# Kernel tuning notes

Hardware: AMD Instinct MI355X
Metric: run time of the kernel (lower is better)

The kernel has to match this reference:

```python
import jax, jax.numpy as jnp
import numpy as np


def conv3x3(x, w):
    # x: [B,C,H,W], w: [O,I,3,3], stride 1, pad 1, no bias
    return jax.lax.conv_general_dilated(
        x, w, window_strides=(1, 1), padding=[(1, 1), (1, 1)],
        dimension_numbers=("NCHW", "OIHW", "NCHW"))


def deform_conv2d(x, offset, w):
    """torchvision-style DeformConv2d: k=3, stride=1, pad=1, dilation=1,
    1 offset group, no bias. x:[B,C,H,W], offset:[B,18,H,W] (dy,dx pairs
    per kernel tap, k = kh*3+kw), w:[O,C,3,3]. Zero padding outside."""
    B, C, H, W = x.shape
    K = 9
    dy = offset[:, 0::2]  # [B,9,H,W]
    dx = offset[:, 1::2]
    kh = (jnp.arange(K) // 3 - 1).astype(x.dtype)[None, :, None, None]
    kw = (jnp.arange(K) % 3 - 1).astype(x.dtype)[None, :, None, None]
    hh = jnp.arange(H, dtype=x.dtype)[None, None, :, None]
    ww = jnp.arange(W, dtype=x.dtype)[None, None, None, :]
    py = hh + kh + dy  # sampling y coord, [B,9,H,W]
    px = ww + kw + dx
    y0 = jnp.floor(py)
    x0 = jnp.floor(px)
    wy = py - y0
    wx = px - x0
    x_hwc = jnp.transpose(x, (0, 2, 3, 1))  # [B,H,W,C]
    b_idx = jnp.arange(B)[:, None, None, None]

    def gather(yi, xi):
        valid = (yi >= 0) & (yi <= H - 1) & (xi >= 0) & (xi <= W - 1)
        yc = jnp.clip(yi, 0, H - 1).astype(jnp.int32)
        xc = jnp.clip(xi, 0, W - 1).astype(jnp.int32)
        v = x_hwc[b_idx, yc, xc]  # [B,9,H,W,C]
        return v * valid[..., None].astype(x.dtype)

    v00 = gather(y0, x0)
    v01 = gather(y0, x0 + 1)
    v10 = gather(y0 + 1, x0)
    v11 = gather(y0 + 1, x0 + 1)
    wy = wy[..., None]
    wx = wx[..., None]
    sampled = (v00 * (1 - wy) * (1 - wx) + v01 * (1 - wy) * wx
               + v10 * wy * (1 - wx) + v11 * wy * wx)  # [B,9,H,W,C]
    wk = w.reshape(w.shape[0], w.shape[1], K)  # [O,C,9]
    return jnp.einsum("bkhwc,ock->bohw", sampled, wk)


def setup_inputs() -> dict:
    key = jax.random.key(0)
    ks = jax.random.split(key, 6)
    B, C, H, W = 2, 128, 128, 128
    s = 0.05  # small init so learned offsets stay in a realistic range
    return {
        "input_features": jax.random.normal(ks[0], (B, C, H, W), jnp.float32),
        "reference_features": jax.random.normal(ks[1], (B, C, H, W), jnp.float32),
        "w_est1": jax.random.normal(ks[2], (C, 2 * C, 3, 3), jnp.float32) * s,
        "w_est2": jax.random.normal(ks[3], (C, C, 3, 3), jnp.float32) * s,
        "w_off": jax.random.normal(ks[4], (18, C, 3, 3), jnp.float32) * s,
        "w_def": jax.random.normal(ks[5], (C, C, 3, 3), jnp.float32) * s,
    }


def reference(input_features, reference_features, w_est1, w_est2, w_off, w_def):
    # concat input+reference features along channel dim
    feat = jnp.concatenate([input_features, reference_features], axis=1)  # [B,2C,H,W]
    # dynamic offset estimator: 2-layer 3x3 conv stack 2C->C->C with ReLU
    est = jax.nn.relu(conv3x3(feat, w_est1))
    est = jax.nn.relu(conv3x3(est, w_est2))
    # offset head: C -> 2*9 offsets per pixel
    offset = conv3x3(est, w_off)  # [B,18,H,W]
    # deformable conv over the reference features
    return deform_conv2d(reference_features, offset, w_def)
```

## Files before the change

kernel.cpp:

```cpp
#include <hip/hip_runtime.h>

typedef _Float16 f16;
typedef __attribute__((ext_vector_type(8))) _Float16 f16x8;
typedef __attribute__((ext_vector_type(4))) float f32x4;
typedef __attribute__((ext_vector_type(4))) int i32x4;


__device__ __forceinline__ void pack_conv(const float* __restrict__ src, f16* __restrict__ dst,
                                          long idx, int C) {
  int ci3 = idx & 7;
  int g = (idx >> 3) & 3;
  long t = idx >> 5;
  int o = (int)(t & 63); t >>= 6;
  int kx = (int)(t % 3); t /= 3;
  int nb = (int)(t & 1); t >>= 1;
  int nkc = C >> 5;
  int cc = (int)(t % nkc);
  int ky = (int)(t / nkc);
  int og = nb * 64 + o;
  int c = (cc << 5) + ((g ^ ((o >> 1) & 3)) << 3) + ci3;
  dst[idx] = (f16)src[(((size_t)og * C + c) * 3 + ky) * 3 + kx];
}

__device__ __forceinline__ void halo_zero(f16* __restrict__ buf, long e) {
  int c = (int)(e & 127);
  long t = e >> 7;
  int b = (int)(t / 516);
  int p = (int)(t % 516);
  int y, x;
  if (p < 130)      { y = 0;   x = p; }
  else if (p < 260) { y = 129; x = p - 130; }
  else if (p < 388) { x = 0;   y = p - 259; }
  else              { x = 129; y = p - 387; }
  buf[((size_t)(b * 130 + y) * 130 + x) * 128 + c] = (f16)0.f;
}

__global__ __launch_bounds__(256) void init_k(const float* __restrict__ x, const float* __restrict__ ref,
                                              const float* __restrict__ w1, const float* __restrict__ w2,
                                              const float* __restrict__ woff, const float* __restrict__ wdef,
                                              f16* __restrict__ W1p, f16* __restrict__ W2p,
                                              f16* __restrict__ Woffp, f16* __restrict__ Wdefp,
                                              f16* __restrict__ xP, f16* __restrict__ refP,
                                              f16* __restrict__ est1, f16* __restrict__ est2) {
  __shared__ __align__(16) f16 T[64][40];
  int tid = threadIdx.x;
  if (blockIdx.x < 4096) {
    int bi = blockIdx.x;
    int row = bi & 255, wseg = (bi >> 8) & 1, chunk = bi >> 9;
    int b = row >> 7, h = row & 127;
    int w0 = wseg * 64;
    const float* src = (chunk < 4) ? x : ref;
    f16* dstp = (chunk < 4) ? xP : refP;
    int c0 = (chunk & 3) * 32;
#pragma unroll
    for (int i = 0; i < 2; ++i) {
      int idx = tid + i * 256;
      int c = idx >> 4, g = idx & 15;
      const float4 v = *(const float4*)(src + (((size_t)(b * 128 + c0 + c)) * 128 + h) * 128 + w0 + g * 4);
      T[g * 4 + 0][c] = (f16)v.x;
      T[g * 4 + 1][c] = (f16)v.y;
      T[g * 4 + 2][c] = (f16)v.z;
      T[g * 4 + 3][c] = (f16)v.w;
    }
    __syncthreads();
    int w = tid >> 2, g = tid & 3;
    f16x8 o = *(const f16x8*)&T[w][g * 8];
    *(f16x8*)(dstp + ((size_t)(b * 130 + h + 1) * 130 + w0 + w + 1) * 128 + c0 + g * 8) = o;
    return;
  }
  long idx = (long)(blockIdx.x - 4096) * 256 + tid;
  if (idx < 294912) { pack_conv(w1, W1p, idx, 256); return; }
  idx -= 294912;
  if (idx < 147456) { pack_conv(w2, W2p, idx, 128); return; }
  idx -= 147456;
  if (idx < 36864) {
    int ci3 = (int)(idx & 7);
    int g = (int)((idx >> 3) & 3);
    int o = (int)((idx >> 5) & 31);
    int t2 = (int)(idx >> 10);
    int kx = t2 % 3; t2 /= 3;
    int cc = t2 & 3, ky = t2 >> 2;
    int c = (cc << 5) + ((g ^ ((o >> 1) & 3)) << 3) + ci3;
    Woffp[idx] = (o < 18) ? (f16)woff[(((size_t)o * 128 + c) * 3 + ky) * 3 + kx] : (f16)0.f;
    return;
  }
  idx -= 36864;
  if (idx < 147456) {
    int j = (int)(idx & 7);
    int ln = (int)((idx >> 3) & 63);
    int ofr = (int)((idx >> 9) & 7);
    int cc = (int)((idx >> 12) & 3);
    int t = (int)(idx >> 14);
    int o = ofr * 16 + (ln & 15);
    int c = cc * 32 + (ln >> 4) * 8 + j;
    Wdefp[idx] = (f16)wdef[(((size_t)o * 128 + c) * 3 + t / 3) * 3 + t % 3];
    return;
  }
  idx -= 147456;
  if (idx < 132096) { halo_zero(xP, idx); return; }
  idx -= 132096;
  if (idx < 132096) { halo_zero(refP, idx); return; }
  idx -= 132096;
  if (idx < 132096) { halo_zero(est1, idx); return; }
  idx -= 132096;
  if (idx < 132096) halo_zero(est2, idx);
}

template <int NKC>
__global__ __launch_bounds__(256, 2) void conv_k(const f16* __restrict__ src0,
                                                 const f16* __restrict__ src1,
                                                 const f16* __restrict__ Wp,
                                                 f16* __restrict__ dst) {
  constexpr int S = 3 * NKC;
  const int j = blockIdx.x;
  const int xcd = j & 7, ji = j >> 3;
  const int row = xcd * 32 + (ji & 31);
  const int nb = ji >> 5;
  const int b = row >> 7, h = row & 127;
  __shared__ __align__(16) f16 As[3][130][32];
  __shared__ __align__(16) f16 Bs[3][3][64][32];
  const int tid = threadIdx.x;
  const int lane = tid & 63, wave = tid >> 6;
  const int l16 = lane & 15, quad = lane >> 4;
  const int wmB = wave * 32;
  f32x4 acc[2][4] = {};

  i32x4 ra0, ra1, ra2, rb0, rb1, rb2;

  auto stage_load = [&](int s) {
    int ky = s / NKC, cc = s % NKC;
    const f16* sp = (NKC == 8 && cc >= 4) ? src1 : src0;
    int c0 = (NKC == 8 ? (cc & 3) : cc) * 32;
    const f16* abase = sp + ((size_t)(b * 130 + h + ky) * 130) * 128 + c0;
    {
      int ch = tid;
      int xx = ch >> 2, g = ch & 3;
      ra0 = *(const i32x4*)(abase + (size_t)xx * 128 + ((g ^ ((xx >> 1) & 3)) << 3));
    }
    {
      int ch = 256 + tid;
      int xx = ch >> 2, g = ch & 3;
      ra1 = *(const i32x4*)(abase + (size_t)xx * 128 + ((g ^ ((xx >> 1) & 3)) << 3));
    }
    if (tid < 8) {
      int ch = 512 + tid;
      int xx = ch >> 2, g = ch & 3;
      ra2 = *(const i32x4*)(abase + (size_t)xx * 128 + ((g ^ ((xx >> 1) & 3)) << 3));
    }
    const f16* bbase = Wp + (size_t)((ky * NKC + cc) * 2 + nb) * (3 * 64 * 32);
    rb0 = *(const i32x4*)(bbase + (size_t)tid * 8);
    rb1 = *(const i32x4*)(bbase + (size_t)(256 + tid) * 8);
    rb2 = *(const i32x4*)(bbase + (size_t)(512 + tid) * 8);
  };
  auto stage_write = [&](int buf) {
    *(i32x4*)((char*)&As[buf][0][0] + tid * 16) = ra0;
    *(i32x4*)((char*)&As[buf][0][0] + (256 + tid) * 16) = ra1;
    if (tid < 8)
      *(i32x4*)((char*)&As[buf][0][0] + (512 + tid) * 16) = ra2;
    *(i32x4*)((char*)&Bs[buf][0][0][0] + tid * 16) = rb0;
    *(i32x4*)((char*)&Bs[buf][0][0][0] + (256 + tid) * 16) = rb1;
    *(i32x4*)((char*)&Bs[buf][0][0][0] + (512 + tid) * 16) = rb2;
  };

  stage_load(0);
  stage_write(0);
  stage_load(1);
  __syncthreads();
  for (int s = 0; s < S; ++s) {
    const int buf = s % 3;
#pragma unroll
    for (int kx = 0; kx < 3; ++kx) {
      f16x8 bf[4];
#pragma unroll
      for (int j2 = 0; j2 < 4; ++j2) {
        int o = j2 * 16 + l16;
        bf[j2] = *(const f16x8*)&Bs[buf][kx][o][(quad ^ ((o >> 1) & 3)) << 3];
      }
#pragma unroll
      for (int i = 0; i < 2; ++i) {
        int xx = wmB + i * 16 + l16 + kx;
        f16x8 a = *(const f16x8*)&As[buf][xx][(quad ^ ((xx >> 1) & 3)) << 3];
#pragma unroll
        for (int j2 = 0; j2 < 4; ++j2)
          acc[i][j2] = __builtin_amdgcn_mfma_f32_16x16x32_f16(a, bf[j2], acc[i][j2], 0, 0, 0);
      }
    }
    if (s + 1 < S) stage_write((s + 1) % 3);
    if (s + 2 < S) stage_load(s + 2);
    __syncthreads();
  }
#pragma unroll
  for (int i = 0; i < 2; ++i)
#pragma unroll
    for (int j2 = 0; j2 < 4; ++j2) {
      int o = nb * 64 + j2 * 16 + l16;
#pragma unroll
      for (int rr = 0; rr < 4; ++rr) {
        int m = wmB + i * 16 + quad * 4 + rr;
        float v = fmaxf(acc[i][j2][rr], 0.f);
        dst[((size_t)(b * 130 + h + 1) * 130 + m + 1) * 128 + o] = (f16)v;
      }
    }
}

__global__ __launch_bounds__(256, 2) void deform_k(const f16* __restrict__ refP,
                                                   const f16* __restrict__ est2,
                                                   const f16* __restrict__ Woffp,
                                                   const f16* __restrict__ Wdefp,
                                                   float* __restrict__ out) {
  const int j = blockIdx.x;
  const int xcd = j & 7, ji = j >> 3;
  const int row = xcd * 32 + (ji & 31);
  const int tile = ji >> 5;
  const int b = row >> 7, h = row & 127;
  __shared__ __align__(16) char smem[32768];
  __shared__ __align__(16) float offs[64][32];
  __shared__ int4 meta[9][64];
  f16 (*Ss)[64][128] = (f16(*)[64][128])smem;
  f16 (*As3)[66][32] = (f16(*)[66][32])smem;
  f16 (*Bs3)[3][32][32] = (f16(*)[3][32][32])(smem + 12672);
  const int tid = threadIdx.x;
  const int lane = tid & 63, wave = tid >> 6;
  const int l16 = lane & 15, quad = lane >> 4;
  const int x0 = tile * 64;

  {
    i32x4 ra0, ra1, rb0, rb1;
    auto sl = [&](int s) {
      int ky = s >> 2, cc = s & 3;
      const f16* abase = est2 + (((size_t)(b * 130 + h + ky)) * 130 + x0) * 128 + cc * 32;
      {
        int ch = tid;
        int xx = ch >> 2, g = ch & 3;
        ra0 = *(const i32x4*)(abase + (size_t)xx * 128 + ((g ^ ((xx >> 1) & 3)) << 3));
      }
      if (tid < 8) {
        int ch = 256 + tid;
        int xx = ch >> 2, g = ch & 3;
        ra1 = *(const i32x4*)(abase + (size_t)xx * 128 + ((g ^ ((xx >> 1) & 3)) << 3));
      }
      const f16* bbase = Woffp + (size_t)(ky * 4 + cc) * (3 * 32 * 32);
      rb0 = *(const i32x4*)(bbase + (size_t)tid * 8);
      if (tid < 128) rb1 = *(const i32x4*)(bbase + (size_t)(256 + tid) * 8);
    };
    auto sw = [&](int buf) {
      *(i32x4*)((char*)&As3[buf][0][0] + tid * 16) = ra0;
      if (tid < 8)
        *(i32x4*)((char*)&As3[buf][0][0] + (256 + tid) * 16) = ra1;
      *(i32x4*)((char*)&Bs3[buf][0][0][0] + tid * 16) = rb0;
      if (tid < 128)
        *(i32x4*)((char*)&Bs3[buf][0][0][0] + (256 + tid) * 16) = rb1;
    };
    f32x4 oacc[2] = {};
    sl(0); sw(0); sl(1);
    __syncthreads();
    for (int s = 0; s < 12; ++s) {
      const int buf = s % 3;
#pragma unroll
      for (int kx = 0; kx < 3; ++kx) {
        f16x8 bf[2];
#pragma unroll
        for (int j2 = 0; j2 < 2; ++j2) {
          int o = j2 * 16 + l16;
          bf[j2] = *(const f16x8*)&Bs3[buf][kx][o][(quad ^ ((o >> 1) & 3)) << 3];
        }
        int xx = wave * 16 + l16 + kx;
        f16x8 a = *(const f16x8*)&As3[buf][xx][(quad ^ ((xx >> 1) & 3)) << 3];
#pragma unroll
        for (int j2 = 0; j2 < 2; ++j2)
          oacc[j2] = __builtin_amdgcn_mfma_f32_16x16x32_f16(a, bf[j2], oacc[j2], 0, 0, 0);
      }
      if (s + 1 < 12) sw((s + 1) % 3);
      if (s + 2 < 12) sl(s + 2);
      __syncthreads();
    }
#pragma unroll
    for (int j2 = 0; j2 < 2; ++j2)
#pragma unroll
      for (int rr = 0; rr < 4; ++rr)
        offs[wave * 16 + quad * 4 + rr][j2 * 16 + l16] = oacc[j2][rr];
  }
  __syncthreads();

  for (int e = tid; e < 576; e += 256) {
    int t = e >> 6, p = e & 63;
    int wg = tile * 64 + p;
    float dy = offs[p][2 * t], dx = offs[p][2 * t + 1];
    float py = (float)(h + t / 3 - 1) + dy;
    float px = (float)(wg + t % 3 - 1) + dx;
    float fy = floorf(py), fx = floorf(px);
    meta[t][p] = make_int4((int)fy, (int)fx, __float_as_int(py - fy), __float_as_int(px - fx));
  }

  const int sp_p = tid >> 2, sp_cg = tid & 3;
  f16x8 v00[4], v01[4], v10[4], v11[4];
  f16 h00, h01, h10, h11;

  auto sample_issue = [&](int t) {
    int4 mt = meta[t][sp_p];
    int yp = mt.x + 1, xp = mt.y + 1;
    float wy = __int_as_float(mt.z), wx = __int_as_float(mt.w);
    bool y0v = (unsigned)yp < 130u, y1v = (unsigned)(yp + 1) < 130u;
    bool x0v = (unsigned)xp < 130u, x1v = (unsigned)(xp + 1) < 130u;
    int cy0 = y0v ? yp : 0, cy1 = y1v ? yp + 1 : 0;
    int cx0 = x0v ? xp : 0, cx1 = x1v ? xp + 1 : 0;
    float u0 = (1.f - wy) * (y0v ? 1.f : 0.f), u1 = wy * (y1v ? 1.f : 0.f);
    float s0 = (1.f - wx) * (x0v ? 1.f : 0.f), s1 = wx * (x1v ? 1.f : 0.f);
    h00 = (f16)(u0 * s0); h01 = (f16)(u0 * s1);
    h10 = (f16)(u1 * s0); h11 = (f16)(u1 * s1);
    const size_t bb = (size_t)b * 130;
    const f16* p00 = refP + ((bb + cy0) * 130 + cx0) * 128 + sp_cg * 32;
    const f16* p01 = refP + ((bb + cy0) * 130 + cx1) * 128 + sp_cg * 32;
    const f16* p10 = refP + ((bb + cy1) * 130 + cx0) * 128 + sp_cg * 32;
    const f16* p11 = refP + ((bb + cy1) * 130 + cx1) * 128 + sp_cg * 32;
#pragma unroll
    for (int q = 0; q < 4; ++q) {
      v00[q] = *(const f16x8*)(p00 + q * 8);
      v01[q] = *(const f16x8*)(p01 + q * 8);
      v10[q] = *(const f16x8*)(p10 + q * 8);
      v11[q] = *(const f16x8*)(p11 + q * 8);
    }
  };
  auto sample_finish = [&](int buf) {
#pragma unroll
    for (int q = 0; q < 4; ++q) {
      f16x8 rb = v00[q] * h00 + v01[q] * h01 + v10[q] * h10 + v11[q] * h11;
      int c = sp_cg * 4 + q;
      *(f16x8*)&Ss[buf][sp_p][(c ^ (sp_p & 7)) << 3] = rb;
    }
  };

  f32x4 acc[2][4] = {};
  f16x8 af0[4][2], af1[4][2];
  __syncthreads();
  sample_issue(0);
  sample_finish(0);
  sample_issue(1);
#pragma unroll
  for (int cc = 0; cc < 4; ++cc)
#pragma unroll
    for (int i = 0; i < 2; ++i)
      af0[cc][i] = *(const f16x8*)(Wdefp +
          ((((size_t)0 * 4 + cc) * 8 + wave * 2 + i) * 64 + lane) * 8);
  __syncthreads();
#pragma unroll
  for (int t = 0; t < 9; ++t) {
    if (t < 8) {
#pragma unroll
      for (int cc = 0; cc < 4; ++cc)
#pragma unroll
        for (int i = 0; i < 2; ++i) {
          f16x8 w = *(const f16x8*)(Wdefp +
              ((((size_t)(t + 1) * 4 + cc) * 8 + wave * 2 + i) * 64 + lane) * 8);
          if (t & 1) af0[cc][i] = w; else af1[cc][i] = w;
        }
    }
    const int buf = t & 1;
    __builtin_amdgcn_s_setprio(1);
#pragma unroll
    for (int cc = 0; cc < 4; ++cc) {
      f16x8 bf[4];
#pragma unroll
      for (int j2 = 0; j2 < 4; ++j2) {
        int p = j2 * 16 + l16;
        bf[j2] = *(const f16x8*)&Ss[buf][p][((cc * 4 + quad) ^ (p & 7)) << 3];
      }
#pragma unroll
      for (int i = 0; i < 2; ++i)
#pragma unroll
        for (int j2 = 0; j2 < 4; ++j2)
          acc[i][j2] = __builtin_amdgcn_mfma_f32_16x16x32_f16(
              (t & 1) ? af1[cc][i] : af0[cc][i], bf[j2], acc[i][j2], 0, 0, 0);
    }
    __builtin_amdgcn_s_setprio(0);
    if (t < 8) sample_finish((t + 1) & 1);
    if (t < 7) sample_issue(t + 2);
    __syncthreads();
  }
#pragma unroll
  for (int i = 0; i < 2; ++i)
#pragma unroll
    for (int rr = 0; rr < 4; ++rr) {
      int o = wave * 32 + i * 16 + quad * 4 + rr;
#pragma unroll
      for (int j2 = 0; j2 < 4; ++j2) {
        int wg = tile * 64 + j2 * 16 + l16;
        out[((size_t)(b * 128 + o) * 128 + h) * 128 + wg] = acc[i][j2][rr];
      }
    }
}

extern "C" void kernel_launch(void* const* d_in, const int* in_sizes, int n_in,
                              void* d_out, int out_size, void* d_ws, size_t ws_size,
                              hipStream_t stream) {
  const float* x = (const float*)d_in[0];
  const float* ref = (const float*)d_in[1];
  const float* w1 = (const float*)d_in[2];
  const float* w2 = (const float*)d_in[3];
  const float* woff = (const float*)d_in[4];
  const float* wdef = (const float*)d_in[5];
  float* out = (float*)d_out;
  char* ws = (char*)d_ws;
  f16* xP = (f16*)(ws + 0);
  f16* refP = (f16*)(ws + 8652800);
  f16* est1 = (f16*)(ws + 17305600);
  f16* est2 = (f16*)(ws + 25958400);
  f16* W1p = (f16*)(ws + 34611200);
  f16* W2p = (f16*)(ws + 35201024);
  f16* Woffp = (f16*)(ws + 35495936);
  f16* Wdefp = (f16*)(ws + 35569664);

  init_k<<<dim3(8608), 256, 0, stream>>>(x, ref, w1, w2, woff, wdef,
                                         W1p, W2p, Woffp, Wdefp, xP, refP, est1, est2);
  conv_k<8><<<dim3(512), 256, 0, stream>>>(xP, refP, W1p, est1);
  conv_k<4><<<dim3(512), 256, 0, stream>>>(est1, est1, W2p, est2);
  deform_k<<<dim3(512), 256, 0, stream>>>(refP, est2, Woffp, Wdefp, out);
}
```

Before: 160.5 us.

## Load conv weight fragments directly from global into registers, drop LDS B tile

The conv kernel no longer stages the weight tile through shared memory. Each lane now reads its MFMA B fragments straight from global memory into registers, using two register sets that alternate so the next stage's weights are prefetched while the current stage computes. This removes the LDS writes and reads for weights and shrinks shared memory use. In exchange it adds more register pressure, and each wave issues redundant global loads of the same weights, served from cache.

```diff
diff --git a/kernel.cpp b/kernel.cpp
--- a/kernel.cpp
+++ b/kernel.cpp
@@ -118,16 +118,15 @@
   const int nb = ji >> 5;
   const int b = row >> 7, h = row & 127;
   __shared__ __align__(16) f16 As[3][130][32];
-  __shared__ __align__(16) f16 Bs[3][3][64][32];
   const int tid = threadIdx.x;
   const int lane = tid & 63, wave = tid >> 6;
   const int l16 = lane & 15, quad = lane >> 4;
   const int wmB = wave * 32;
   f32x4 acc[2][4] = {};
 
-  i32x4 ra0, ra1, ra2, rb0, rb1, rb2;
-
-  auto stage_load = [&](int s) {
+  i32x4 ra0, ra1, ra2;
+
+  auto loadA = [&](int s) {
     int ky = s / NKC, cc = s % NKC;
     const f16* sp = (NKC == 8 && cc >= 4) ? src1 : src0;
     int c0 = (NKC == 8 ? (cc & 3) : cc) * 32;
@@ -147,47 +146,56 @@
       int xx = ch >> 2, g = ch & 3;
       ra2 = *(const i32x4*)(abase + (size_t)xx * 128 + ((g ^ ((xx >> 1) & 3)) << 3));
     }
-    const f16* bbase = Wp + (size_t)((ky * NKC + cc) * 2 + nb) * (3 * 64 * 32);
-    rb0 = *(const i32x4*)(bbase + (size_t)tid * 8);
-    rb1 = *(const i32x4*)(bbase + (size_t)(256 + tid) * 8);
-    rb2 = *(const i32x4*)(bbase + (size_t)(512 + tid) * 8);
-  };
-  auto stage_write = [&](int buf) {
+  };
+  auto writeA = [&](int buf) {
     *(i32x4*)((char*)&As[buf][0][0] + tid * 16) = ra0;
     *(i32x4*)((char*)&As[buf][0][0] + (256 + tid) * 16) = ra1;
     if (tid < 8)
       *(i32x4*)((char*)&As[buf][0][0] + (512 + tid) * 16) = ra2;
-    *(i32x4*)((char*)&Bs[buf][0][0][0] + tid * 16) = rb0;
-    *(i32x4*)((char*)&Bs[buf][0][0][0] + (256 + tid) * 16) = rb1;
-    *(i32x4*)((char*)&Bs[buf][0][0][0] + (512 + tid) * 16) = rb2;
-  };
-
-  stage_load(0);
-  stage_write(0);
-  stage_load(1);
-  __syncthreads();
-  for (int s = 0; s < S; ++s) {
-    const int buf = s % 3;
-#pragma unroll
-    for (int kx = 0; kx < 3; ++kx) {
-      f16x8 bf[4];
+  };
+  auto loadB = [&](int s, f16x8 (&bf)[3][4]) {
+    int ky = s / NKC, cc = s % NKC;
+    const f16* bbase = Wp + (size_t)((ky * NKC + cc) * 2 + nb) * (3 * 64 * 32);
+#pragma unroll
+    for (int kx = 0; kx < 3; ++kx)
 #pragma unroll
       for (int j2 = 0; j2 < 4; ++j2) {
         int o = j2 * 16 + l16;
-        bf[j2] = *(const f16x8*)&Bs[buf][kx][o][(quad ^ ((o >> 1) & 3)) << 3];
-      }
+        bf[kx][j2] = *(const f16x8*)(bbase + kx * (64 * 32) + o * 32 +
+                                     ((quad ^ ((o >> 1) & 3)) << 3));
+      }
+  };
+  auto compute = [&](int buf, f16x8 (&bf)[3][4]) {
+#pragma unroll
+    for (int kx = 0; kx < 3; ++kx)
 #pragma unroll
       for (int i = 0; i < 2; ++i) {
         int xx = wmB + i * 16 + l16 + kx;
         f16x8 a = *(const f16x8*)&As[buf][xx][(quad ^ ((xx >> 1) & 3)) << 3];
 #pragma unroll
         for (int j2 = 0; j2 < 4; ++j2)
-          acc[i][j2] = __builtin_amdgcn_mfma_f32_16x16x32_f16(a, bf[j2], acc[i][j2], 0, 0, 0);
-      }
-    }
-    if (s + 1 < S) stage_write((s + 1) % 3);
-    if (s + 2 < S) stage_load(s + 2);
+          acc[i][j2] = __builtin_amdgcn_mfma_f32_16x16x32_f16(a, bf[kx][j2], acc[i][j2], 0, 0, 0);
+      }
+  };
+
+  f16x8 bfA[3][4], bfB[3][4];
+  loadA(0); writeA(0);
+  loadA(1);
+  loadB(0, bfA);
+  __syncthreads();
+  for (int s = 0; s < S; s += 2) {
+    if (s + 1 < S) loadB(s + 1, bfB);
+    compute(s % 3, bfA);
+    if (s + 1 < S) writeA((s + 1) % 3);
+    if (s + 2 < S) loadA(s + 2);
     __syncthreads();
+    if (s + 1 < S) {
+      if (s + 2 < S) loadB(s + 2, bfA);
+      compute((s + 1) % 3, bfB);
+      if (s + 2 < S) writeA((s + 2) % 3);
+      if (s + 3 < S) loadA(s + 3);
+      __syncthreads();
+    }
   }
 #pragma unroll
   for (int i = 0; i < 2; ++i)
```

Result: slower. 167.0 us (+4.1%).
